# Performance work log

Measured on AMD Instinct MI355X. Metric: run time of the kernel, lower is better.

Reference implementation:

```python
import jax, jax.numpy as jnp
import numpy as np

V = 32          # number_variables
DEG = 12        # degree
ORDER = 3       # spline_order (cubic)
N_BASIS = DEG + ORDER - 1  # 14, rows of params
LO, HI = -15.0, 15.0       # polynomial_range[:, 0]
EPS = 1e-6


def make_knots():
    dist = (HI - LO) / (DEG - 1)
    k = DEG + 2 * ORDER
    return jnp.linspace(LO - ORDER * dist, HI + ORDER * dist, k, dtype=jnp.float32)


def bspline_basis(x, knots, order):
    # x: [N, P] -> basis: [N, P, N_BASIS] via Cox-de Boor recursion (Naive_Basis)
    xk = x[..., None]
    b = ((xk >= knots[:-1]) & (xk < knots[1:])).astype(x.dtype)  # degree-0, [N,P,K-1]
    t = knots
    for k in range(1, order + 1):
        left = (xk - t[:-(k + 1)]) / (t[k:-1] - t[:-(k + 1)])
        right = (t[k + 1:] - xk) / (t[k + 1:] - t[1:-k])
        b = left * b[..., :-1] + right * b[..., 1:]
    return b  # [N, P, K-1-order] == [N, P, N_BASIS]


def setup_inputs() -> dict:
    key = jax.random.key(0)
    k1, k2 = jax.random.split(key)
    num_lambdas = V * (V - 1) // 2  # 496
    inp = jax.random.normal(k1, (16384, V), dtype=jnp.float32)
    log_d = jnp.zeros((16384, V), dtype=jnp.float32)
    params = 0.001 * jnp.ones((N_BASIS, num_lambdas), dtype=jnp.float32)
    return {"input": inp, "log_d": log_d, "params": params}


def reference(input, log_d, params):
    n = input.shape[0]
    knots = make_knots()
    rows, cols = np.tril_indices(V, -1)  # matches torch.tril_indices(V, V, offset=-1)
    rows = jnp.asarray(rows); cols = jnp.asarray(cols)
    # clamp into half-open spline support for valid degree-0 basis
    x = jnp.clip(input, LO, HI - EPS)
    xs = x[:, cols]                                  # [N, P] per-pair covariate values
    basis = bspline_basis(xs, knots, ORDER)          # [N, P, N_BASIS]
    lam = jnp.einsum('npk,kp->np', basis, params)    # [N, P] lambda values
    # lower-triangular lambda matrix: identity + strict lower entries
    lm = jnp.broadcast_to(jnp.eye(V, dtype=input.dtype), (n, V, V))
    lm = lm.at[:, rows, cols].set(lam)
    out = jnp.einsum('nvc,nc->nv', lm, input)        # bmm(lambda_matrix, input)
    # ridge penalties on spline coefficients (penalize_towards=0)
    d2 = jnp.diff(params, n=2, axis=0)
    d1 = jnp.diff(params, n=1, axis=0)
    second_pen = jnp.sum(d2 ** 2)
    first_pen = jnp.sum(d1 ** 2)
    param_pen = jnp.sum(params ** 2)
    return out, lm, second_pen, first_pen, param_pen
```

## Files before the change

### kernel.cpp

```cpp
#include <hip/hip_runtime.h>

#define VDIM   32
#define NPAIR  496
#define NBASIS 14
#define NPARAM (NBASIS * NPAIR)
#define NINT   11
#define ROWS   8
#define LROW   544

typedef float f32x4 __attribute__((ext_vector_type(4)));

__device__ __forceinline__ int seg_of(int v) {
    int m = v - 1;
    if (m <= 0) return 0;
    int q = m >> 2, r = m & 3;
    return 4 * (2 * q * (q + 1) + r * (q + 1));
}

__global__ __launch_bounds__(256) void Decorrelation_prep(
    const float* __restrict__ params,
    f32x4* __restrict__ ptv,
    float* __restrict__ pens)
{
    const int tid = threadIdx.x;
    const int b   = blockIdx.x;
    if (b < NINT) {
        const int i = b;
        for (int p = tid; p < NPAIR; p += 256) {
            f32x4 w = { params[(i    ) * NPAIR + p],
                        params[(i + 1) * NPAIR + p],
                        params[(i + 2) * NPAIR + p],
                        params[(i + 3) * NPAIR + p] };
            ptv[i * NPAIR + p] = w;
        }
    } else {
        float s2 = 0.f, s1 = 0.f, sp = 0.f;
        for (int idx = tid; idx < NPARAM; idx += 256) {
            const float a = params[idx];
            sp += a * a;
            if (idx < NPARAM - NPAIR) {
                const float bb = params[idx + NPAIR];
                const float d1 = bb - a;
                s1 += d1 * d1;
                if (idx < NPARAM - 2 * NPAIR) {
                    const float cc = params[idx + 2 * NPAIR];
                    const float d2 = cc - 2.f * bb + a;
                    s2 += d2 * d2;
                }
            }
        }
        #pragma unroll
        for (int off = 32; off > 0; off >>= 1) {
            s2 += __shfl_down(s2, off);
            s1 += __shfl_down(s1, off);
            sp += __shfl_down(sp, off);
        }
        __shared__ float ws[3][4];
        const int lane = tid & 63, wid = tid >> 6;
        if (lane == 0) { ws[0][wid] = s2; ws[1][wid] = s1; ws[2][wid] = sp; }
        __syncthreads();
        if (tid == 0) {
            pens[0] = ws[0][0] + ws[0][1] + ws[0][2] + ws[0][3];
            pens[1] = ws[1][0] + ws[1][1] + ws[1][2] + ws[1][3];
            pens[2] = ws[2][0] + ws[2][1] + ws[2][2] + ws[2][3];
        }
    }
}

__global__ __launch_bounds__(256, 6) void Decorrelation_35270271435435_kernel(
    const float* __restrict__ input,
    const f32x4* __restrict__ ptv,
    float* __restrict__ out,
    float* __restrict__ lm,
    int N)
{
    __shared__ float lam[ROWS][LROW];

    const int tid  = threadIdx.x;
    const int wave = tid >> 6;
    const int lane = tid & 63;
    const int n0   = blockIdx.x * ROWS;

    int  oo[8], cc[8], pp[8];
    bool act[8];
    #pragma unroll
    for (int k = 0; k < 8; ++k) {
        const int p = lane + 64 * k;
        act[k] = (p < NPAIR);
        const int pe = act[k] ? p : (NPAIR - 1);
        int v = (int)((1.0f + sqrtf(8.0f * (float)pe + 1.0f)) * 0.5f);
        while (v * (v - 1) / 2 > pe) --v;
        while ((v + 1) * v / 2 <= pe) ++v;
        const int c = pe - v * (v - 1) / 2;
        pp[k] = pe; cc[k] = c; oo[k] = seg_of(v) + c;
    }

    const float dist  = 30.0f / 11.0f;
    const float invd  = 11.0f / 30.0f;
    const float t0    = -15.0f - 3.0f * dist;
    const float sixth = 1.0f / 6.0f;

    #pragma unroll
    for (int rr = 0; rr < 2; ++rr) {
        const int r = wave * 2 + rr;
        const int n = n0 + r;
        if (n >= N) break;
        const float* xrow = input + n * VDIM;
        #pragma unroll
        for (int k = 0; k < 8; ++k) {
            const float xi = xrow[cc[k]];
            float x = fminf(fmaxf(xi, -15.0f), 15.0f - 1e-6f);
            float u = (x - t0) * invd;
            int   i = (int)floorf(u);
            i = min(13, max(3, i));
            const float uu  = u - (float)i;
            const float om  = 1.0f - uu;
            const float uu2 = uu * uu, uu3 = uu2 * uu;
            const float w0 = om * om * om * sixth;
            const float w1 = (3.0f * uu3 - 6.0f * uu2 + 4.0f) * sixth;
            const float w2 = (-3.0f * uu3 + 3.0f * uu2 + 3.0f * uu + 1.0f) * sixth;
            const float w3 = uu3 * sixth;
            const f32x4 q  = ptv[(i - 3) * NPAIR + pp[k]];
            const float lv = w0 * q.x + w1 * q.y + w2 * q.z + w3 * q.w;
            if (act[k]) lam[r][oo[k]] = lv;
        }
    }

    #pragma unroll
    for (int rr = 0; rr < 2; ++rr) {
        const int r = wave * 2 + rr;
        const int n = n0 + r;
        if (n >= N) break;
        const float* xrow  = input + n * VDIM;
        float*       lmrow = lm + (size_t)n * (VDIM * VDIM);
        #pragma unroll
        for (int j = 0; j < 4; ++j) {
            const int v  = j * 8 + (lane >> 3);
            const int c0 = (lane & 7) << 2;
            const f32x4 lq = *(const f32x4*)&lam[r][seg_of(v) + c0];
            const f32x4 xq = *(const f32x4*)(xrow + c0);
            float vals[4];
            float partial = 0.0f;
            #pragma unroll
            for (int t = 0; t < 4; ++t) {
                const int c = c0 + t;
                const float lv = (t == 0) ? lq.x : (t == 1) ? lq.y : (t == 2) ? lq.z : lq.w;
                const float xv = (t == 0) ? xq.x : (t == 1) ? xq.y : (t == 2) ? xq.z : xq.w;
                const float val = (c < v) ? lv : ((c == v) ? 1.0f : 0.0f);
                vals[t] = val;
                partial += val * xv;
            }
            f32x4 f4 = { vals[0], vals[1], vals[2], vals[3] };
            *(f32x4*)(lmrow + j * 256 + lane * 4) = f4;

            partial += __shfl_down(partial, 4, 8);
            partial += __shfl_down(partial, 2, 8);
            partial += __shfl_down(partial, 1, 8);
            if ((lane & 7) == 0) out[n * VDIM + v] = partial;
        }
    }
}

extern "C" void kernel_launch(void* const* d_in, const int* in_sizes, int n_in,
                              void* d_out, int out_size, void* d_ws, size_t ws_size,
                              hipStream_t stream) {
    const float* input  = (const float*)d_in[0];
    const float* params = (const float*)d_in[2];
    const int N = in_sizes[0] / VDIM;

    float* out  = (float*)d_out;
    float* lm   = out + (size_t)N * VDIM;
    float* pens = lm + (size_t)N * VDIM * VDIM;

    f32x4* ptv = (f32x4*)d_ws;

    Decorrelation_prep<<<NINT + 1, 256, 0, stream>>>(params, ptv, pens);

    const int nb = (N + ROWS - 1) / ROWS;
    Decorrelation_35270271435435_kernel<<<nb, 256, 0, stream>>>(
        input, ptv, out, lm, N);
}
```

Baseline: 102.4 us.

## Fuse prep and penalty into main kernel, one row per wave

Removes the separate prep kernel that packed params into float4 windows. The main kernel now reads four scalar params directly and computes the penalties in block 0. Each wave handles one row instead of two, so twice as many blocks are launched, and the occupancy hint rises from 6 to 8. This saves a launch and a serial dependency, at the cost of four scattered scalar loads in place of one vector load, and extra work in block 0.

```diff
diff --git a/kernel.cpp b/kernel.cpp
--- a/kernel.cpp
+++ b/kernel.cpp
@@ -4,8 +4,6 @@
 #define NPAIR  496
 #define NBASIS 14
 #define NPARAM (NBASIS * NPAIR)
-#define NINT   11
-#define ROWS   8
 #define LROW   544
 
 typedef float f32x4 __attribute__((ext_vector_type(4)));
@@ -17,35 +15,97 @@
     return 4 * (2 * q * (q + 1) + r * (q + 1));
 }
 
-__global__ __launch_bounds__(256) void Decorrelation_prep(
+__global__ __launch_bounds__(256, 8) void Decorrelation_35270271435435_kernel(
+    const float* __restrict__ input,
     const float* __restrict__ params,
-    f32x4* __restrict__ ptv,
-    float* __restrict__ pens)
+    float* __restrict__ out,
+    float* __restrict__ lm,
+    float* __restrict__ pens,
+    int N)
 {
-    const int tid = threadIdx.x;
-    const int b   = blockIdx.x;
-    if (b < NINT) {
-        const int i = b;
-        for (int p = tid; p < NPAIR; p += 256) {
-            f32x4 w = { params[(i    ) * NPAIR + p],
-                        params[(i + 1) * NPAIR + p],
-                        params[(i + 2) * NPAIR + p],
-                        params[(i + 3) * NPAIR + p] };
-            ptv[i * NPAIR + p] = w;
+    __shared__ float lam[4][LROW];
+
+    const int tid  = threadIdx.x;
+    const int wave = tid >> 6;
+    const int lane = tid & 63;
+    const int n    = blockIdx.x * 4 + wave;
+
+    const float invd  = 11.0f / 30.0f;
+    const float t0    = -15.0f - 3.0f * (30.0f / 11.0f);
+    const float sixth = 1.0f / 6.0f;
+
+    if (n < N) {
+        const float* xrow = input + n * VDIM;
+
+        for (int k = 0; k < 8; ++k) {
+            const int  p  = lane + (k << 6);
+            const bool a  = (p < NPAIR);
+            const int  pe = a ? p : (NPAIR - 1);
+            int v = (int)((1.0f + sqrtf(8.0f * (float)pe + 1.0f)) * 0.5f);
+            v -= (v * (v - 1) / 2 > pe) ? 1 : 0;
+            v += ((v + 1) * v / 2 <= pe) ? 1 : 0;
+            const int c = pe - v * (v - 1) / 2;
+            const int o = seg_of(v) + c;
+            const float xi = xrow[c];
+            float x = fminf(fmaxf(xi, -15.0f), 15.0f - 1e-6f);
+            float u = (x - t0) * invd;
+            int   i = (int)floorf(u);
+            i = min(13, max(3, i));
+            const float uu  = u - (float)i;
+            const float om  = 1.0f - uu;
+            const float uu2 = uu * uu, uu3 = uu2 * uu;
+            const float w0 = om * om * om * sixth;
+            const float w1 = fmaf(3.0f, uu3, fmaf(-6.0f, uu2, 4.0f)) * sixth;
+            const float w2 = fmaf(-3.0f, uu3, fmaf(3.0f, uu2, fmaf(3.0f, uu, 1.0f))) * sixth;
+            const float w3 = uu3 * sixth;
+            const int b = (i - 3) * NPAIR + pe;
+            const float lv = w0 * params[b]
+                           + w1 * params[b + NPAIR]
+                           + w2 * params[b + 2 * NPAIR]
+                           + w3 * params[b + 3 * NPAIR];
+            if (a) lam[wave][o] = lv;
         }
-    } else {
+
+        float* lmrow = lm + (size_t)n * (VDIM * VDIM);
+        for (int j = 0; j < 4; ++j) {
+            const int v  = j * 8 + (lane >> 3);
+            const int c0 = (lane & 7) << 2;
+            const f32x4 lq = *(const f32x4*)&lam[wave][seg_of(v) + c0];
+            const f32x4 xq = *(const f32x4*)(xrow + c0);
+            float vals[4];
+            float partial = 0.0f;
+            #pragma unroll
+            for (int t = 0; t < 4; ++t) {
+                const int c = c0 + t;
+                const float lv = (t == 0) ? lq.x : (t == 1) ? lq.y : (t == 2) ? lq.z : lq.w;
+                const float xv = (t == 0) ? xq.x : (t == 1) ? xq.y : (t == 2) ? xq.z : xq.w;
+                const float val = (c < v) ? lv : ((c == v) ? 1.0f : 0.0f);
+                vals[t] = val;
+                partial = fmaf(val, xv, partial);
+            }
+            f32x4 f4 = { vals[0], vals[1], vals[2], vals[3] };
+            *(f32x4*)(lmrow + (j << 8) + (lane << 2)) = f4;
+
+            partial += __shfl_down(partial, 4, 8);
+            partial += __shfl_down(partial, 2, 8);
+            partial += __shfl_down(partial, 1, 8);
+            if ((lane & 7) == 0) out[n * VDIM + v] = partial;
+        }
+    }
+
+    if (blockIdx.x == 0) {
         float s2 = 0.f, s1 = 0.f, sp = 0.f;
         for (int idx = tid; idx < NPARAM; idx += 256) {
             const float a = params[idx];
-            sp += a * a;
+            sp = fmaf(a, a, sp);
             if (idx < NPARAM - NPAIR) {
-                const float bb = params[idx + NPAIR];
-                const float d1 = bb - a;
-                s1 += d1 * d1;
+                const float b = params[idx + NPAIR];
+                const float d1 = b - a;
+                s1 = fmaf(d1, d1, s1);
                 if (idx < NPARAM - 2 * NPAIR) {
-                    const float cc = params[idx + 2 * NPAIR];
-                    const float d2 = cc - 2.f * bb + a;
-                    s2 += d2 * d2;
+                    const float c = params[idx + 2 * NPAIR];
+                    const float d2 = c - 2.f * b + a;
+                    s2 = fmaf(d2, d2, s2);
                 }
             }
         }
@@ -56,107 +116,12 @@
             sp += __shfl_down(sp, off);
         }
         __shared__ float ws[3][4];
-        const int lane = tid & 63, wid = tid >> 6;
-        if (lane == 0) { ws[0][wid] = s2; ws[1][wid] = s1; ws[2][wid] = sp; }
+        if (lane == 0) { ws[0][wave] = s2; ws[1][wave] = s1; ws[2][wave] = sp; }
         __syncthreads();
         if (tid == 0) {
             pens[0] = ws[0][0] + ws[0][1] + ws[0][2] + ws[0][3];
             pens[1] = ws[1][0] + ws[1][1] + ws[1][2] + ws[1][3];
             pens[2] = ws[2][0] + ws[2][1] + ws[2][2] + ws[2][3];
-        }
-    }
-}
-
-__global__ __launch_bounds__(256, 6) void Decorrelation_35270271435435_kernel(
-    const float* __restrict__ input,
-    const f32x4* __restrict__ ptv,
-    float* __restrict__ out,
-    float* __restrict__ lm,
-    int N)
-{
-    __shared__ float lam[ROWS][LROW];
-
-    const int tid  = threadIdx.x;
-    const int wave = tid >> 6;
-    const int lane = tid & 63;
-    const int n0   = blockIdx.x * ROWS;
-
-    int  oo[8], cc[8], pp[8];
-    bool act[8];
-    #pragma unroll
-    for (int k = 0; k < 8; ++k) {
-        const int p = lane + 64 * k;
-        act[k] = (p < NPAIR);
-        const int pe = act[k] ? p : (NPAIR - 1);
-        int v = (int)((1.0f + sqrtf(8.0f * (float)pe + 1.0f)) * 0.5f);
-        while (v * (v - 1) / 2 > pe) --v;
-        while ((v + 1) * v / 2 <= pe) ++v;
-        const int c = pe - v * (v - 1) / 2;
-        pp[k] = pe; cc[k] = c; oo[k] = seg_of(v) + c;
-    }
-
-    const float dist  = 30.0f / 11.0f;
-    const float invd  = 11.0f / 30.0f;
-    const float t0    = -15.0f - 3.0f * dist;
-    const float sixth = 1.0f / 6.0f;
-
-    #pragma unroll
-    for (int rr = 0; rr < 2; ++rr) {
-        const int r = wave * 2 + rr;
-        const int n = n0 + r;
-        if (n >= N) break;
-        const float* xrow = input + n * VDIM;
-        #pragma unroll
-        for (int k = 0; k < 8; ++k) {
-            const float xi = xrow[cc[k]];
-            float x = fminf(fmaxf(xi, -15.0f), 15.0f - 1e-6f);
-            float u = (x - t0) * invd;
-            int   i = (int)floorf(u);
-            i = min(13, max(3, i));
-            const float uu  = u - (float)i;
-            const float om  = 1.0f - uu;
-            const float uu2 = uu * uu, uu3 = uu2 * uu;
-            const float w0 = om * om * om * sixth;
-            const float w1 = (3.0f * uu3 - 6.0f * uu2 + 4.0f) * sixth;
-            const float w2 = (-3.0f * uu3 + 3.0f * uu2 + 3.0f * uu + 1.0f) * sixth;
-            const float w3 = uu3 * sixth;
-            const f32x4 q  = ptv[(i - 3) * NPAIR + pp[k]];
-            const float lv = w0 * q.x + w1 * q.y + w2 * q.z + w3 * q.w;
-            if (act[k]) lam[r][oo[k]] = lv;
-        }
-    }
-
-    #pragma unroll
-    for (int rr = 0; rr < 2; ++rr) {
-        const int r = wave * 2 + rr;
-        const int n = n0 + r;
-        if (n >= N) break;
-        const float* xrow  = input + n * VDIM;
-        float*       lmrow = lm + (size_t)n * (VDIM * VDIM);
-        #pragma unroll
-        for (int j = 0; j < 4; ++j) {
-            const int v  = j * 8 + (lane >> 3);
-            const int c0 = (lane & 7) << 2;
-            const f32x4 lq = *(const f32x4*)&lam[r][seg_of(v) + c0];
-            const f32x4 xq = *(const f32x4*)(xrow + c0);
-            float vals[4];
-            float partial = 0.0f;
-            #pragma unroll
-            for (int t = 0; t < 4; ++t) {
-                const int c = c0 + t;
-                const float lv = (t == 0) ? lq.x : (t == 1) ? lq.y : (t == 2) ? lq.z : lq.w;
-                const float xv = (t == 0) ? xq.x : (t == 1) ? xq.y : (t == 2) ? xq.z : xq.w;
-                const float val = (c < v) ? lv : ((c == v) ? 1.0f : 0.0f);
-                vals[t] = val;
-                partial += val * xv;
-            }
-            f32x4 f4 = { vals[0], vals[1], vals[2], vals[3] };
-            *(f32x4*)(lmrow + j * 256 + lane * 4) = f4;
-
-            partial += __shfl_down(partial, 4, 8);
-            partial += __shfl_down(partial, 2, 8);
-            partial += __shfl_down(partial, 1, 8);
-            if ((lane & 7) == 0) out[n * VDIM + v] = partial;
         }
     }
 }
@@ -172,11 +137,7 @@
     float* lm   = out + (size_t)N * VDIM;
     float* pens = lm + (size_t)N * VDIM * VDIM;
 
-    f32x4* ptv = (f32x4*)d_ws;
-
-    Decorrelation_prep<<<NINT + 1, 256, 0, stream>>>(params, ptv, pens);
-
-    const int nb = (N + ROWS - 1) / ROWS;
+    const int nb = (N + 3) / 4;
     Decorrelation_35270271435435_kernel<<<nb, 256, 0, stream>>>(
-        input, ptv, out, lm, N);
+        input, params, out, lm, pens, N);
 }
```

After: 103.2 us. About the same (+0.8%).
